# Optimization experiments

Hardware: AMD Instinct MI355X
Metric: run time of the kernel (lower is better)

## Reference

```python
import jax, jax.numpy as jnp
import numpy as np

B, S, H, I, E, K = 2, 512, 768, 3072, 8, 1
LB_COEF = 0.01


def _xavier(key, shape, fan_in, fan_out):
    limit = np.sqrt(6.0 / (fan_in + fan_out)).astype(np.float32)
    return jax.random.uniform(key, shape, jnp.float32, -limit, limit)


def setup_inputs() -> dict:
    key = jax.random.key(0)
    k0, k1, k2, k3 = jax.random.split(key, 4)
    return {
        "hidden_states": jax.random.normal(k0, (B, S, H), jnp.float32),
        "gate_w": _xavier(k1, (E, H), H, E),          # nn.Linear(H, E).weight
        "gate_b": jnp.zeros((E,), jnp.float32),
        "w1": _xavier(k2, (E, I, H), H, I),           # per-expert Linear(H, I).weight
        "b1": jnp.zeros((E, I), jnp.float32),
        "w2": _xavier(k3, (E, H, I), I, H),           # per-expert Linear(I, H).weight
        "b2": jnp.zeros((E, H), jnp.float32),
    }


def reference(hidden_states, gate_w, gate_b, w1, b1, w2, b2):
    b, s, h = hidden_states.shape
    x = hidden_states.reshape(-1, h)                      # [T, H]
    gate_logits = x @ gate_w.T + gate_b                   # [T, E]
    top_vals, top_idx = jax.lax.top_k(gate_logits, K)     # [T, K]
    # softmax over the (single) selected logit in fp32 -> all ones, kept for fidelity
    gate_weights = jax.nn.softmax(top_vals.astype(jnp.float32), axis=-1)  # [T, K]

    # load balancing loss (torch.var is unbiased, ddof=1)
    gate_mean = gate_logits.mean(axis=0)                  # [E]
    gate_var = gate_logits.var(axis=0, ddof=1)            # [E]
    lb_loss = LB_COEF * (gate_var / (gate_mean ** 2 + 1e-8)).mean()

    # dense per-expert FFN (exact math; combine picks the routed expert)
    hmid = jnp.einsum('th,eih->tei', x, w1) + b1          # [T, E, I]
    hmid = jax.nn.gelu(hmid, approximate=False)           # torch nn.GELU (erf)
    y = jnp.einsum('tei,ehi->teh', hmid, w2) + b2         # [T, E, H]

    sel = top_idx[:, 0]                                   # [T]
    y_sel = jnp.take_along_axis(y, sel[:, None, None], axis=1)[:, 0]  # [T, H]
    out = y_sel * gate_weights[:, 0:1]                    # weight == 1.0 for k=1
    return out.reshape(b, s, h), lb_loss
```

## Files before the change

kernel.cpp:

```cpp
#include <hip/hip_runtime.h>
#include <hip/hip_bf16.h>
#include <math.h>

#define Hdim 768
#define Idim 3072
#define Tn   1024
#define En   8
#define LD1  72
#define LD2  136

using v4f     = __attribute__((ext_vector_type(4))) float;
using short8  = __attribute__((ext_vector_type(8))) short;
using short4v = __attribute__((ext_vector_type(4))) short;

__device__ inline unsigned short f2bf(float f) {
    unsigned u = __float_as_uint(f);
    u += 0x7fffu + ((u >> 16) & 1u);
    return (unsigned short)(u >> 16);
}
__device__ inline short4v pack4(float4 v) {
    return short4v{ (short)f2bf(v.x), (short)f2bf(v.y), (short)f2bf(v.z), (short)f2bf(v.w) };
}
__device__ __forceinline__ void gl2lds16(const unsigned short* g, unsigned short* l) {
    __builtin_amdgcn_global_load_lds(
        (const __attribute__((address_space(1))) void*)g,
        (__attribute__((address_space(3))) void*)l, 16, 0, 0);
}

__global__ __launch_bounds__(256) void gate_kernel(
    const float* __restrict__ x, const float* __restrict__ gw, const float* __restrict__ gb,
    float* __restrict__ gsum, float* __restrict__ gsumsq,
    int* __restrict__ count, int* __restrict__ sel)
{
    __shared__ float gws[8 * 772];
    __shared__ float lg[8][8];
    int tid = threadIdx.x;
    long t0 = (long)blockIdx.x * 8;
    for (int i = tid; i < 8 * 768; i += 256) gws[(i / 768) * 772 + (i % 768)] = gw[i];
    __syncthreads();

    int tok = tid >> 5, e = (tid >> 2) & 7, qr = tid & 3;
    const float4* xp = (const float4*)(x + (t0 + tok) * Hdim) + qr * 48;
    const float4* gp = (const float4*)(gws + e * 772) + qr * 48;
    float a0 = 0.f, a1 = 0.f;
#pragma unroll 8
    for (int i = 0; i < 48; i += 2) {
        float4 xa = xp[i], ga = gp[i], xc = xp[i + 1], gc = gp[i + 1];
        a0 += xa.x * ga.x + xa.y * ga.y + xa.z * ga.z + xa.w * ga.w;
        a1 += xc.x * gc.x + xc.y * gc.y + xc.z * gc.z + xc.w * gc.w;
    }
    float acc = a0 + a1;
    acc += __shfl_xor(acc, 1);
    acc += __shfl_xor(acc, 2);
    if (qr == 0) lg[tok][e] = acc + gb[e];
    __syncthreads();

    if (tid < 8) {
        float best = lg[tid][0]; int bi = 0;
        for (int j = 1; j < 8; j++) { float v = lg[tid][j]; if (v > best) { best = v; bi = j; } }
        sel[t0 + tid] = bi;
        atomicAdd(&count[bi], 1);
    } else if (tid < 16) {
        int e2 = tid - 8;
        float s = 0.f, ss = 0.f;
        for (int t2 = 0; t2 < 8; t2++) { float v = lg[t2][e2]; s += v; ss += v * v; }
        atomicAdd(&gsum[e2], s);
        atomicAdd(&gsumsq[e2], ss);
    }
}

__global__ void finalize_kernel(const float* __restrict__ gsum, const float* __restrict__ gsumsq,
                                const int* __restrict__ count,
                                int* __restrict__ offsets, int* __restrict__ cursor,
                                float* __restrict__ out_lb)
{
    if (threadIdx.x == 0) {
        float accr = 0.f;
        for (int e = 0; e < 8; e++) {
            float mean = gsum[e] * (1.0f / 1024.0f);
            float var  = (gsumsq[e] - gsum[e] * mean) * (1.0f / 1023.0f);
            accr += var / (mean * mean + 1e-8f);
        }
        out_lb[0] = 0.01f * accr * 0.125f;
        int off = 0;
        for (int e = 0; e < 8; e++) { offsets[e] = off; cursor[e] = off; off += count[e]; }
    }
}

__global__ __launch_bounds__(256) void scatter_kernel(const int* __restrict__ sel,
                                                      int* __restrict__ cursor,
                                                      int* __restrict__ perm)
{
    int t = blockIdx.x * 256 + threadIdx.x;
    if (t < Tn) {
        int e = sel[t];
        int pos = atomicAdd(&cursor[e], 1);
        perm[pos] = t;
    }
}

__global__ __launch_bounds__(256) void gather_x_kernel(const float* __restrict__ x,
                                                       const int* __restrict__ perm,
                                                       unsigned short* __restrict__ xb)
{
    int slot = blockIdx.x * 4 + (threadIdx.x >> 6);
    int lane = threadIdx.x & 63;
    int t = perm[slot];
    const float4* src = (const float4*)(x + (long)t * Hdim);
    unsigned short* dst = xb + (long)slot * Hdim;
#pragma unroll
    for (int i = 0; i < 3; i++) {
        int c = lane + 64 * i;
        *(short4v*)(dst + c * 4) = pack4(src[c]);
    }
}

__global__ __launch_bounds__(256) void init_out_kernel(const float* __restrict__ b2,
                                                       const int* __restrict__ sel,
                                                       float* __restrict__ out)
{
    int t = blockIdx.x;
    int h = blockIdx.y * 256 + threadIdx.x;
    out[(long)t * Hdim + h] = b2[sel[t] * Hdim + h];
}

__global__ __launch_bounds__(256) void gemm1_kernel(
    const unsigned short* __restrict__ xb, const float* __restrict__ w1, const float* __restrict__ b1,
    const int* __restrict__ count, const int* __restrict__ offsets,
    unsigned short* __restrict__ hmid)
{
    int e = blockIdx.z;
    int nloc = count[e];
    int m0 = blockIdx.y << 7;
    if (m0 >= nloc) return;
    int n0 = blockIdx.x << 5;
    int off = offsets[e];

    __shared__ __align__(16) unsigned short As[128 * 64];
    __shared__ __align__(16) unsigned short Bs[32 * LD1];

    int tid = threadIdx.x;
    int lane = tid & 63, wave = tid >> 6;
    int quad = lane >> 4, l16 = lane & 15;
    int wm = wave << 5;

    const unsigned short* aG[4];
    unsigned short* aL[4];
#pragma unroll
    for (int i = 0; i < 4; i++) {
        int p = (wave * 4 + i) * 64 + lane;
        int row = p >> 3;
        int kc = (p & 7) ^ (row & 7);
        int m = m0 + row; int mm = m < nloc ? m : nloc - 1;
        aG[i] = xb + (long)(off + mm) * Hdim + kc * 8;
        aL[i] = (unsigned short*)As + p * 8;
    }
    int kq = tid & 15, rb = tid >> 4;
    const float* bp0 = w1 + ((long)e * Idim + n0 + rb) * Hdim + kq * 4;
    const float* bp1 = bp0 + (long)16 * Hdim;

    v4f acc[2][2];
#pragma unroll
    for (int i = 0; i < 2; i++)
#pragma unroll
        for (int j = 0; j < 2; j++) acc[i][j] = (v4f){0.f, 0.f, 0.f, 0.f};

    float4 nb0 = *(const float4*)bp0;
    float4 nb1 = *(const float4*)bp1;

    for (int kb = 0; kb < Hdim; kb += 64) {
        __syncthreads();
#pragma unroll
        for (int i = 0; i < 4; i++) gl2lds16(aG[i] + kb, aL[i]);
        *(short4v*)(Bs + rb * LD1 + kq * 4)        = pack4(nb0);
        *(short4v*)(Bs + (rb + 16) * LD1 + kq * 4) = pack4(nb1);
        __syncthreads();
        if (kb + 64 < Hdim) {
            nb0 = *(const float4*)(bp0 + kb + 64);
            nb1 = *(const float4*)(bp1 + kb + 64);
        }
#pragma unroll
        for (int s = 0; s < 2; s++) {
            short8 af[2], bf2[2];
#pragma unroll
            for (int i = 0; i < 2; i++) {
                int r = wm + i * 16 + l16;
                af[i] = *(const short8*)(As + r * 64 + (((s * 4 + quad) ^ (r & 7)) * 8));
            }
#pragma unroll
            for (int j = 0; j < 2; j++)
                bf2[j] = *(const short8*)(Bs + (j * 16 + l16) * LD1 + s * 32 + quad * 8);
#pragma unroll
            for (int i = 0; i < 2; i++)
#pragma unroll
                for (int j = 0; j < 2; j++)
                    acc[i][j] = __builtin_amdgcn_mfma_f32_16x16x32_bf16(af[i], bf2[j], acc[i][j], 0, 0, 0);
        }
    }

#pragma unroll
    for (int i = 0; i < 2; i++) {
        int mr = wm + i * 16 + quad * 4;
#pragma unroll
        for (int r = 0; r < 4; r++) {
            int m = m0 + mr + r;
            if (m >= nloc) continue;
            long slot = off + m;
#pragma unroll
            for (int j = 0; j < 2; j++) {
                int n = n0 + j * 16 + l16;
                float v = acc[i][j][r] + b1[e * Idim + n];
                float g = 0.5f * v * (1.0f + erff(v * 0.70710678118654752f));
                hmid[slot * Idim + n] = f2bf(g);
            }
        }
    }
}

__global__ __launch_bounds__(256) void gemm2_kernel(
    const unsigned short* __restrict__ hmid, const float* __restrict__ w2,
    const int* __restrict__ count, const int* __restrict__ offsets,
    const int* __restrict__ perm, float* __restrict__ out)
{
    int e = blockIdx.z;
    int nloc = count[e];
    int m0 = blockIdx.y << 7;
    if (m0 >= nloc) return;
    int bx = blockIdx.x;
    int n0 = (bx % 24) << 5;
    long kbase = (long)(bx / 24) * 768;
    int off = offsets[e];

    __shared__ __align__(16) unsigned short As[128 * 128];
    __shared__ __align__(16) unsigned short Bs[32 * LD2];

    int tid = threadIdx.x;
    int lane = tid & 63, wave = tid >> 6;
    int quad = lane >> 4, l16 = lane & 15;
    int wm = wave << 5;

    const unsigned short* aG[8];
    unsigned short* aL[8];
#pragma unroll
    for (int i = 0; i < 8; i++) {
        int p = (wave * 8 + i) * 64 + lane;
        int row = p >> 4;
        int kc = (p & 15) ^ (row & 15);
        int m = m0 + row; int mm = m < nloc ? m : nloc - 1;
        aG[i] = hmid + (long)(off + mm) * Idim + kbase + kc * 8;
        aL[i] = (unsigned short*)As + p * 8;
    }
    int kq5 = tid & 31, rb8 = tid >> 5;
    const float* bp[4];
#pragma unroll
    for (int s = 0; s < 4; s++)
        bp[s] = w2 + ((long)e * Hdim + n0 + rb8 + 8 * s) * Idim + kbase + kq5 * 4;

    v4f acc[2][2];
#pragma unroll
    for (int i = 0; i < 2; i++)
#pragma unroll
        for (int j = 0; j < 2; j++) acc[i][j] = (v4f){0.f, 0.f, 0.f, 0.f};

    float4 nb[4];
#pragma unroll
    for (int s = 0; s < 4; s++) nb[s] = *(const float4*)bp[s];

    for (int kb = 0; kb < 768; kb += 128) {
        __syncthreads();
#pragma unroll
        for (int i = 0; i < 8; i++) gl2lds16(aG[i] + kb, aL[i]);
#pragma unroll
        for (int s = 0; s < 4; s++)
            *(short4v*)(Bs + (rb8 + 8 * s) * LD2 + kq5 * 4) = pack4(nb[s]);
        __syncthreads();
        if (kb + 128 < 768) {
#pragma unroll
            for (int s = 0; s < 4; s++) nb[s] = *(const float4*)(bp[s] + kb + 128);
        }
#pragma unroll
        for (int s = 0; s < 4; s++) {
            short8 af[2], bf2[2];
#pragma unroll
            for (int i = 0; i < 2; i++) {
                int r = wm + i * 16 + l16;
                af[i] = *(const short8*)(As + r * 128 + (((s * 4 + quad) ^ (r & 15)) * 8));
            }
#pragma unroll
            for (int j = 0; j < 2; j++)
                bf2[j] = *(const short8*)(Bs + (j * 16 + l16) * LD2 + s * 32 + quad * 8);
#pragma unroll
            for (int i = 0; i < 2; i++)
#pragma unroll
                for (int j = 0; j < 2; j++)
                    acc[i][j] = __builtin_amdgcn_mfma_f32_16x16x32_bf16(af[i], bf2[j], acc[i][j], 0, 0, 0);
        }
    }

#pragma unroll
    for (int i = 0; i < 2; i++) {
        int mr = wm + i * 16 + quad * 4;
#pragma unroll
        for (int r = 0; r < 4; r++) {
            int m = m0 + mr + r;
            if (m >= nloc) continue;
            int t = perm[off + m];
#pragma unroll
            for (int j = 0; j < 2; j++) {
                int n = n0 + j * 16 + l16;
                atomicAdd(out + (long)t * Hdim + n, acc[i][j][r]);
            }
        }
    }
}

extern "C" void kernel_launch(void* const* d_in, const int* in_sizes, int n_in,
                              void* d_out, int out_size, void* d_ws, size_t ws_size,
                              hipStream_t stream)
{
    const float* x  = (const float*)d_in[0];
    const float* gw = (const float*)d_in[1];
    const float* gb = (const float*)d_in[2];
    const float* w1 = (const float*)d_in[3];
    const float* b1 = (const float*)d_in[4];
    const float* w2 = (const float*)d_in[5];
    const float* b2 = (const float*)d_in[6];
    float* out = (float*)d_out;

    float* gsum    = (float*)d_ws;
    float* gsumsq  = gsum + 8;
    int*   count   = (int*)d_ws + 16;
    int*   offsets = (int*)d_ws + 24;
    int*   cursor  = (int*)d_ws + 32;
    int*   sel     = (int*)d_ws + 40;
    int*   perm    = (int*)d_ws + 40 + 1024;
    unsigned short* xb   = (unsigned short*)((char*)d_ws + 8704);
    unsigned short* hmid = (unsigned short*)((char*)d_ws + 8704 + (size_t)Tn * Hdim * 2);

    hipMemsetAsync(d_ws, 0, 160, stream);
    gate_kernel<<<128, 256, 0, stream>>>(x, gw, gb, gsum, gsumsq, count, sel);
    finalize_kernel<<<1, 64, 0, stream>>>(gsum, gsumsq, count, offsets, cursor, out + (long)Tn * Hdim);
    scatter_kernel<<<4, 256, 0, stream>>>(sel, cursor, perm);
    gather_x_kernel<<<256, 256, 0, stream>>>(x, perm, xb);
    init_out_kernel<<<dim3(Tn, 3), 256, 0, stream>>>(b2, sel, out);
    gemm1_kernel<<<dim3(96, 2, 8), 256, 0, stream>>>(xb, w1, b1, count, offsets, hmid);
    gemm2_kernel<<<dim3(96, 2, 8), 256, 0, stream>>>(hmid, w2, count, offsets, perm, out);
}
```

Measured before the change: 240.5 us.

## Fuse routing kernels and halve GEMM M-tile to 64 rows

Merges the finalize and scatter kernels into one 1024-thread block that uses a shared-memory cursor. Merges the x-gather and bias-initialisation kernels into one. Together these cut kernel launches and global atomics. Both expert GEMMs now use 64-row M tiles with one 16-row MFMA strip per wave and twice as many y-blocks. This gives more parallel blocks for the uneven per-expert token counts, but each block reuses less of the fp32 weight tile, so weight reads and bf16 conversions roughly double.

```diff
diff --git a/kernel.cpp b/kernel.cpp
--- a/kernel.cpp
+++ b/kernel.cpp
@@ -69,12 +69,15 @@
     }
 }
 
-__global__ void finalize_kernel(const float* __restrict__ gsum, const float* __restrict__ gsumsq,
-                                const int* __restrict__ count,
-                                int* __restrict__ offsets, int* __restrict__ cursor,
-                                float* __restrict__ out_lb)
-{
-    if (threadIdx.x == 0) {
+__global__ __launch_bounds__(1024) void finscat_kernel(
+    const float* __restrict__ gsum, const float* __restrict__ gsumsq,
+    const int* __restrict__ count, int* __restrict__ offsets,
+    const int* __restrict__ sel, int* __restrict__ perm,
+    float* __restrict__ out_lb)
+{
+    __shared__ int lcur[8];
+    int tid = threadIdx.x;
+    if (tid == 0) {
         float accr = 0.f;
         for (int e = 0; e < 8; e++) {
             float mean = gsum[e] * (1.0f / 1024.0f);
@@ -83,45 +86,33 @@
         }
         out_lb[0] = 0.01f * accr * 0.125f;
         int off = 0;
-        for (int e = 0; e < 8; e++) { offsets[e] = off; cursor[e] = off; off += count[e]; }
-    }
-}
-
-__global__ __launch_bounds__(256) void scatter_kernel(const int* __restrict__ sel,
-                                                      int* __restrict__ cursor,
-                                                      int* __restrict__ perm)
-{
-    int t = blockIdx.x * 256 + threadIdx.x;
-    if (t < Tn) {
-        int e = sel[t];
-        int pos = atomicAdd(&cursor[e], 1);
-        perm[pos] = t;
-    }
-}
-
-__global__ __launch_bounds__(256) void gather_x_kernel(const float* __restrict__ x,
-                                                       const int* __restrict__ perm,
-                                                       unsigned short* __restrict__ xb)
+        for (int e = 0; e < 8; e++) { offsets[e] = off; lcur[e] = off; off += count[e]; }
+    }
+    __syncthreads();
+    int e = sel[tid];
+    int pos = atomicAdd(&lcur[e], 1);
+    perm[pos] = tid;
+}
+
+__global__ __launch_bounds__(256) void gather_init_kernel(
+    const float* __restrict__ x, const float* __restrict__ b2,
+    const int* __restrict__ perm, const int* __restrict__ sel,
+    unsigned short* __restrict__ xb, float* __restrict__ out)
 {
     int slot = blockIdx.x * 4 + (threadIdx.x >> 6);
     int lane = threadIdx.x & 63;
     int t = perm[slot];
+    int e = sel[t];
     const float4* src = (const float4*)(x + (long)t * Hdim);
+    const float4* bsrc = (const float4*)(b2 + (long)e * Hdim);
     unsigned short* dst = xb + (long)slot * Hdim;
+    float4* odst = (float4*)(out + (long)t * Hdim);
 #pragma unroll
     for (int i = 0; i < 3; i++) {
         int c = lane + 64 * i;
         *(short4v*)(dst + c * 4) = pack4(src[c]);
-    }
-}
-
-__global__ __launch_bounds__(256) void init_out_kernel(const float* __restrict__ b2,
-                                                       const int* __restrict__ sel,
-                                                       float* __restrict__ out)
-{
-    int t = blockIdx.x;
-    int h = blockIdx.y * 256 + threadIdx.x;
-    out[(long)t * Hdim + h] = b2[sel[t] * Hdim + h];
+        odst[c] = bsrc[c];
+    }
 }
 
 __global__ __launch_bounds__(256) void gemm1_kernel(
@@ -131,24 +122,24 @@
 {
     int e = blockIdx.z;
     int nloc = count[e];
-    int m0 = blockIdx.y << 7;
+    int m0 = blockIdx.y << 6;
     if (m0 >= nloc) return;
     int n0 = blockIdx.x << 5;
     int off = offsets[e];
 
-    __shared__ __align__(16) unsigned short As[128 * 64];
+    __shared__ __align__(16) unsigned short As[64 * 64];
     __shared__ __align__(16) unsigned short Bs[32 * LD1];
 
     int tid = threadIdx.x;
     int lane = tid & 63, wave = tid >> 6;
     int quad = lane >> 4, l16 = lane & 15;
-    int wm = wave << 5;
-
-    const unsigned short* aG[4];
-    unsigned short* aL[4];
-#pragma unroll
-    for (int i = 0; i < 4; i++) {
-        int p = (wave * 4 + i) * 64 + lane;
+    int wm = wave << 4;
+
+    const unsigned short* aG[2];
+    unsigned short* aL[2];
+#pragma unroll
+    for (int i = 0; i < 2; i++) {
+        int p = (wave * 2 + i) * 64 + lane;
         int row = p >> 3;
         int kc = (p & 7) ^ (row & 7);
         int m = m0 + row; int mm = m < nloc ? m : nloc - 1;
@@ -159,11 +150,9 @@
     const float* bp0 = w1 + ((long)e * Idim + n0 + rb) * Hdim + kq * 4;
     const float* bp1 = bp0 + (long)16 * Hdim;
 
-    v4f acc[2][2];
-#pragma unroll
-    for (int i = 0; i < 2; i++)
-#pragma unroll
-        for (int j = 0; j < 2; j++) acc[i][j] = (v4f){0.f, 0.f, 0.f, 0.f};
+    v4f acc[2];
+    acc[0] = (v4f){0.f, 0.f, 0.f, 0.f};
+    acc[1] = (v4f){0.f, 0.f, 0.f, 0.f};
 
     float4 nb0 = *(const float4*)bp0;
     float4 nb1 = *(const float4*)bp1;
@@ -171,7 +160,7 @@
     for (int kb = 0; kb < Hdim; kb += 64) {
         __syncthreads();
 #pragma unroll
-        for (int i = 0; i < 4; i++) gl2lds16(aG[i] + kb, aL[i]);
+        for (int i = 0; i < 2; i++) gl2lds16(aG[i] + kb, aL[i]);
         *(short4v*)(Bs + rb * LD1 + kq * 4)        = pack4(nb0);
         *(short4v*)(Bs + (rb + 16) * LD1 + kq * 4) = pack4(nb1);
         __syncthreads();
@@ -181,38 +170,30 @@
         }
 #pragma unroll
         for (int s = 0; s < 2; s++) {
-            short8 af[2], bf2[2];
-#pragma unroll
-            for (int i = 0; i < 2; i++) {
-                int r = wm + i * 16 + l16;
-                af[i] = *(const short8*)(As + r * 64 + (((s * 4 + quad) ^ (r & 7)) * 8));
-            }
+            int r = wm + l16;
+            short8 af = *(const short8*)(As + r * 64 + (((s * 4 + quad) ^ (r & 7)) * 8));
+            short8 bf2[2];
 #pragma unroll
             for (int j = 0; j < 2; j++)
                 bf2[j] = *(const short8*)(Bs + (j * 16 + l16) * LD1 + s * 32 + quad * 8);
 #pragma unroll
-            for (int i = 0; i < 2; i++)
-#pragma unroll
-                for (int j = 0; j < 2; j++)
-                    acc[i][j] = __builtin_amdgcn_mfma_f32_16x16x32_bf16(af[i], bf2[j], acc[i][j], 0, 0, 0);
-        }
-    }
-
-#pragma unroll
-    for (int i = 0; i < 2; i++) {
-        int mr = wm + i * 16 + quad * 4;
-#pragma unroll
-        for (int r = 0; r < 4; r++) {
-            int m = m0 + mr + r;
-            if (m >= nloc) continue;
-            long slot = off + m;
-#pragma unroll
-            for (int j = 0; j < 2; j++) {
-                int n = n0 + j * 16 + l16;
-                float v = acc[i][j][r] + b1[e * Idim + n];
-                float g = 0.5f * v * (1.0f + erff(v * 0.70710678118654752f));
-                hmid[slot * Idim + n] = f2bf(g);
-            }
+            for (int j = 0; j < 2; j++)
+                acc[j] = __builtin_amdgcn_mfma_f32_16x16x32_bf16(af, bf2[j], acc[j], 0, 0, 0);
+        }
+    }
+
+    int mr = wm + quad * 4;
+#pragma unroll
+    for (int r = 0; r < 4; r++) {
+        int m = m0 + mr + r;
+        if (m >= nloc) continue;
+        long slot = off + m;
+#pragma unroll
+        for (int j = 0; j < 2; j++) {
+            int n = n0 + j * 16 + l16;
+            float v = acc[j][r] + b1[e * Idim + n];
+            float g = 0.5f * v * (1.0f + erff(v * 0.70710678118654752f));
+            hmid[slot * Idim + n] = f2bf(g);
         }
     }
 }
@@ -224,26 +205,26 @@
 {
     int e = blockIdx.z;
     int nloc = count[e];
-    int m0 = blockIdx.y << 7;
+    int m0 = blockIdx.y << 6;
     if (m0 >= nloc) return;
     int bx = blockIdx.x;
     int n0 = (bx % 24) << 5;
     long kbase = (long)(bx / 24) * 768;
     int off = offsets[e];
 
-    __shared__ __align__(16) unsigned short As[128 * 128];
+    __shared__ __align__(16) unsigned short As[64 * 128];
     __shared__ __align__(16) unsigned short Bs[32 * LD2];
 
     int tid = threadIdx.x;
     int lane = tid & 63, wave = tid >> 6;
     int quad = lane >> 4, l16 = lane & 15;
-    int wm = wave << 5;
-
-    const unsigned short* aG[8];
-    unsigned short* aL[8];
-#pragma unroll
-    for (int i = 0; i < 8; i++) {
-        int p = (wave * 8 + i) * 64 + lane;
+    int wm = wave << 4;
+
+    const unsigned short* aG[4];
+    unsigned short* aL[4];
+#pragma unroll
+    for (int i = 0; i < 4; i++) {
+        int p = (wave * 4 + i) * 64 + lane;
         int row = p >> 4;
         int kc = (p & 15) ^ (row & 15);
         int m = m0 + row; int mm = m < nloc ? m : nloc - 1;
@@ -256,11 +237,9 @@
     for (int s = 0; s < 4; s++)
         bp[s] = w2 + ((long)e * Hdim + n0 + rb8 + 8 * s) * Idim + kbase + kq5 * 4;
 
-    v4f acc[2][2];
-#pragma unroll
-    for (int i = 0; i < 2; i++)
-#pragma unroll
-        for (int j = 0; j < 2; j++) acc[i][j] = (v4f){0.f, 0.f, 0.f, 0.f};
+    v4f acc[2];
+    acc[0] = (v4f){0.f, 0.f, 0.f, 0.f};
+    acc[1] = (v4f){0.f, 0.f, 0.f, 0.f};
 
     float4 nb[4];
 #pragma unroll
@@ -269,7 +248,7 @@
     for (int kb = 0; kb < 768; kb += 128) {
         __syncthreads();
 #pragma unroll
-        for (int i = 0; i < 8; i++) gl2lds16(aG[i] + kb, aL[i]);
+        for (int i = 0; i < 4; i++) gl2lds16(aG[i] + kb, aL[i]);
 #pragma unroll
         for (int s = 0; s < 4; s++)
             *(short4v*)(Bs + (rb8 + 8 * s) * LD2 + kq5 * 4) = pack4(nb[s]);
@@ -280,36 +259,28 @@
         }
 #pragma unroll
         for (int s = 0; s < 4; s++) {
-            short8 af[2], bf2[2];
-#pragma unroll
-            for (int i = 0; i < 2; i++) {
-                int r = wm + i * 16 + l16;
-                af[i] = *(const short8*)(As + r * 128 + (((s * 4 + quad) ^ (r & 15)) * 8));
-            }
+            int r = wm + l16;
+            short8 af = *(const short8*)(As + r * 128 + (((s * 4 + quad) ^ (r & 15)) * 8));
+            short8 bf2[2];
 #pragma unroll
             for (int j = 0; j < 2; j++)
                 bf2[j] = *(const short8*)(Bs + (j * 16 + l16) * LD2 + s * 32 + quad * 8);
 #pragma unroll
-            for (int i = 0; i < 2; i++)
-#pragma unroll
-                for (int j = 0; j < 2; j++)
-                    acc[i][j] = __builtin_amdgcn_mfma_f32_16x16x32_bf16(af[i], bf2[j], acc[i][j], 0, 0, 0);
-        }
-    }
-
-#pragma unroll
-    for (int i = 0; i < 2; i++) {
-        int mr = wm + i * 16 + quad * 4;
-#pragma unroll
-        for (int r = 0; r < 4; r++) {
-            int m = m0 + mr + r;
-            if (m >= nloc) continue;
-            int t = perm[off + m];
-#pragma unroll
-            for (int j = 0; j < 2; j++) {
-                int n = n0 + j * 16 + l16;
-                atomicAdd(out + (long)t * Hdim + n, acc[i][j][r]);
-            }
+            for (int j = 0; j < 2; j++)
+                acc[j] = __builtin_amdgcn_mfma_f32_16x16x32_bf16(af, bf2[j], acc[j], 0, 0, 0);
+        }
+    }
+
+    int mr = wm + quad * 4;
+#pragma unroll
+    for (int r = 0; r < 4; r++) {
+        int m = m0 + mr + r;
+        if (m >= nloc) continue;
+        int t = perm[off + m];
+#pragma unroll
+        for (int j = 0; j < 2; j++) {
+            int n = n0 + j * 16 + l16;
+            atomicAdd(out + (long)t * Hdim + n, acc[j][r]);
         }
     }
 }
@@ -331,7 +302,6 @@
     float* gsumsq  = gsum + 8;
     int*   count   = (int*)d_ws + 16;
     int*   offsets = (int*)d_ws + 24;
-    int*   cursor  = (int*)d_ws + 32;
     int*   sel     = (int*)d_ws + 40;
     int*   perm    = (int*)d_ws + 40 + 1024;
     unsigned short* xb   = (unsigned short*)((char*)d_ws + 8704);
@@ -339,10 +309,9 @@
 
     hipMemsetAsync(d_ws, 0, 160, stream);
     gate_kernel<<<128, 256, 0, stream>>>(x, gw, gb, gsum, gsumsq, count, sel);
-    finalize_kernel<<<1, 64, 0, stream>>>(gsum, gsumsq, count, offsets, cursor, out + (long)Tn * Hdim);
-    scatter_kernel<<<4, 256, 0, stream>>>(sel, cursor, perm);
-    gather_x_kernel<<<256, 256, 0, stream>>>(x, perm, xb);
-    init_out_kernel<<<dim3(Tn, 3), 256, 0, stream>>>(b2, sel, out);
-    gemm1_kernel<<<dim3(96, 2, 8), 256, 0, stream>>>(xb, w1, b1, count, offsets, hmid);
-    gemm2_kernel<<<dim3(96, 2, 8), 256, 0, stream>>>(hmid, w2, count, offsets, perm, out);
-}
+    finscat_kernel<<<1, 1024, 0, stream>>>(gsum, gsumsq, count, offsets, sel, perm,
+                                           out + (long)Tn * Hdim);
+    gather_init_kernel<<<256, 256, 0, stream>>>(x, b2, perm, sel, xb, out);
+    gemm1_kernel<<<dim3(96, 4, 8), 256, 0, stream>>>(xb, w1, b1, count, offsets, hmid);
+    gemm2_kernel<<<dim3(96, 4, 8), 256, 0, stream>>>(hmid, w2, count, offsets, perm, out);
+}
```

Measured after the change: 231.2 us. 1.04x faster.
